# Kernel tuning notes

Hardware: AMD Instinct MI355X
Metric: run time of the kernel (lower is better)

Reference implementation:

```python
import jax, jax.numpy as jnp
import numpy as np

TOP_K = 2
UP = 4  # upfeat(disp_4, spg, 4, 4)


def reference(cost, spg):
    """cost: [b,1,D,h,w] raw cost volume; spg: [b,9,4h,4w] superpixel logits.
    Returns disp_1: [b,4h,4w] (eval-mode output of CoExDispProcessor regression)."""
    b, _, D, h, w = cost.shape
    # spx_pred = softmax over the 9 neighbor channels
    prob = jax.nn.softmax(spg, axis=1)  # [b,9,4h,4w]

    # --- topkpool (k=2): sort desc along disparity, take top-k values+indices ---
    c = jnp.moveaxis(cost, 2, -1)  # [b,1,h,w,D]
    vals, ind = jax.lax.top_k(c, TOP_K)  # [b,1,h,w,k], sorted descending
    corr = jax.nn.softmax(vals, axis=-1)
    disp4 = jnp.sum(corr * ind.astype(cost.dtype), axis=-1)  # [b,1,h,w]

    pad = jnp.pad(disp4, ((0, 0), (0, 0), (1, 1), (1, 1)))
    # F.unfold ordering: kernel row-major, channel index = ki*3 + kj
    patches = jnp.stack(
        [pad[:, 0, i:i + h, j:j + w] for i in range(3) for j in range(3)],
        axis=1)  # [b,9,h,w]
    up = jnp.repeat(jnp.repeat(patches, UP, axis=2), UP, axis=3)  # [b,9,4h,4w]
    disp1 = jnp.sum(up * prob, axis=1) * 4.0  # [b,4h,4w], scaled to full-res disparity
    return disp1


def setup_inputs() -> dict:
    key = jax.random.key(0)
    k1, k2 = jax.random.split(key)
    b, D, h, w = 8, 48, 128, 240
    cost = jax.random.normal(k1, (b, 1, D, h, w), dtype=jnp.float32)
    spg = jax.random.normal(k2, (b, 9, 4 * h, 4 * w), dtype=jnp.float32)
    return {"cost": cost, "spg": spg}
```

## Files before the change

### kernel.cpp

```cpp
#include <hip/hip_runtime.h>
#include <math.h>

#define BB 8
#define DD 48
#define HH 128
#define WW 240
#define HW (HH * WW)
#define FH (4 * HH)
#define FW (4 * WW)
#define FHW (FH * FW)

__global__ __launch_bounds__(256) void disp4_kernel(const float* __restrict__ cost,
                                                    float* __restrict__ disp4) {
    int t = blockIdx.x * blockDim.x + threadIdx.x;
    const int WQ = WW / 4;
    if (t >= BB * HH * WQ) return;
    int wq = t % WQ;
    int r  = t / WQ;
    int hy = r % HH;
    int b  = r / HH;

    const float* base = cost + (size_t)b * DD * HW + (size_t)hy * WW + wq * 4;

    float m1[4], m2[4], i1[4], i2[4];
#pragma unroll
    for (int k = 0; k < 4; ++k) { m1[k] = -INFINITY; m2[k] = -INFINITY; i1[k] = 0.f; i2[k] = 0.f; }

    for (int d = 0; d < DD; ++d) {
        float4 v4 = *reinterpret_cast<const float4*>(base + (size_t)d * HW);
        float v[4] = {v4.x, v4.y, v4.z, v4.w};
        float fd = (float)d;
#pragma unroll
        for (int k = 0; k < 4; ++k) {
            if (v[k] > m1[k]) {
                m2[k] = m1[k]; i2[k] = i1[k];
                m1[k] = v[k];  i1[k] = fd;
            } else if (v[k] > m2[k]) {
                m2[k] = v[k];  i2[k] = fd;
            }
        }
    }

    float4 o;
    float out[4];
#pragma unroll
    for (int k = 0; k < 4; ++k) {
        float e = __expf(m2[k] - m1[k]);
        float s = e / (1.f + e);
        out[k] = i1[k] + (i2[k] - i1[k]) * s;
    }
    o.x = out[0]; o.y = out[1]; o.z = out[2]; o.w = out[3];
    *reinterpret_cast<float4*>(disp4 + (size_t)b * HW + (size_t)hy * WW + wq * 4) = o;
}

__global__ __launch_bounds__(256) void upfeat_kernel(const float* __restrict__ spg,
                                                     const float* __restrict__ disp4,
                                                     float* __restrict__ out) {
    int t = blockIdx.x * blockDim.x + threadIdx.x;
    const int XQ = FW / 4;
    if (t >= BB * FH * XQ) return;
    int xq = t % XQ;
    int r  = t / XQ;
    int y  = r % FH;
    int b  = r / FH;
    int hy = y >> 2;

    float p[9];
#pragma unroll
    for (int i = 0; i < 3; ++i) {
#pragma unroll
        for (int j = 0; j < 3; ++j) {
            int cy = hy + i - 1;
            int cx = xq + j - 1;
            bool ok = (cy >= 0) & (cy < HH) & (cx >= 0) & (cx < WW);
            p[i * 3 + j] = ok ? disp4[(size_t)b * HW + (size_t)cy * WW + cx] : 0.f;
        }
    }

    const float* sp = spg + ((size_t)b * 9 * FH + (size_t)y) * FW + xq * 4;
    float s[9][4];
#pragma unroll
    for (int c = 0; c < 9; ++c) {
        float4 v = *reinterpret_cast<const float4*>(sp + (size_t)c * FHW);
        s[c][0] = v.x; s[c][1] = v.y; s[c][2] = v.z; s[c][3] = v.w;
    }

    float o[4];
#pragma unroll
    for (int k = 0; k < 4; ++k) {
        float m = s[0][k];
#pragma unroll
        for (int c = 1; c < 9; ++c) m = fmaxf(m, s[c][k]);
        float num = 0.f, den = 0.f;
#pragma unroll
        for (int c = 0; c < 9; ++c) {
            float e = __expf(s[c][k] - m);
            num = fmaf(e, p[c], num);
            den += e;
        }
        o[k] = 4.f * num / den;
    }

    float4 ov; ov.x = o[0]; ov.y = o[1]; ov.z = o[2]; ov.w = o[3];
    *reinterpret_cast<float4*>(out + ((size_t)b * FH + (size_t)y) * FW + xq * 4) = ov;
}

extern "C" void kernel_launch(void* const* d_in, const int* in_sizes, int n_in,
                              void* d_out, int out_size, void* d_ws, size_t ws_size,
                              hipStream_t stream) {
    const float* cost = (const float*)d_in[0];
    const float* spg  = (const float*)d_in[1];
    float* outp  = (float*)d_out;
    float* disp4 = (float*)d_ws;

    {
        int total = BB * HH * (WW / 4);
        int blocks = (total + 255) / 256;
        disp4_kernel<<<blocks, 256, 0, stream>>>(cost, disp4);
    }
    {
        int total = BB * FH * (FW / 4);
        int blocks = (total + 255) / 256;
        upfeat_kernel<<<blocks, 256, 0, stream>>>(spg, disp4, outp);
    }
}
```

Measured before the change: 258.8 us.

## Use nontemporal loads/stores, 2-wide topk threads with unrolled batched loads

The top-2 kernel now gives each thread two columns instead of four, doubling thread count, and unrolls the disparity loop in groups of eight, issuing all loads first and then doing branchless select updates. Both kernels switch to nontemporal loads, and the upsample kernel also uses a nontemporal store and a fast divide. The aim is more memory-level parallelism and less cache pollution on this bandwidth-bound streaming workload. Risks include narrower 8-byte loads and slightly less precise division.

```diff
diff --git a/kernel.cpp b/kernel.cpp
--- a/kernel.cpp
+++ b/kernel.cpp
@@ -10,47 +10,56 @@
 #define FW (4 * WW)
 #define FHW (FH * FW)
 
+typedef float vf2 __attribute__((ext_vector_type(2)));
+typedef float vf4 __attribute__((ext_vector_type(4)));
+
 __global__ __launch_bounds__(256) void disp4_kernel(const float* __restrict__ cost,
                                                     float* __restrict__ disp4) {
     int t = blockIdx.x * blockDim.x + threadIdx.x;
-    const int WQ = WW / 4;
+    const int WQ = WW / 2;
     if (t >= BB * HH * WQ) return;
     int wq = t % WQ;
     int r  = t / WQ;
     int hy = r % HH;
     int b  = r / HH;
 
-    const float* base = cost + (size_t)b * DD * HW + (size_t)hy * WW + wq * 4;
+    const float* base = cost + (size_t)b * DD * HW + (size_t)hy * WW + wq * 2;
 
-    float m1[4], m2[4], i1[4], i2[4];
+    float m1[2], m2[2], i1[2], i2[2];
 #pragma unroll
-    for (int k = 0; k < 4; ++k) { m1[k] = -INFINITY; m2[k] = -INFINITY; i1[k] = 0.f; i2[k] = 0.f; }
+    for (int k = 0; k < 2; ++k) { m1[k] = -INFINITY; m2[k] = -INFINITY; i1[k] = 0.f; i2[k] = 0.f; }
 
-    for (int d = 0; d < DD; ++d) {
-        float4 v4 = *reinterpret_cast<const float4*>(base + (size_t)d * HW);
-        float v[4] = {v4.x, v4.y, v4.z, v4.w};
-        float fd = (float)d;
 #pragma unroll
-        for (int k = 0; k < 4; ++k) {
-            if (v[k] > m1[k]) {
-                m2[k] = m1[k]; i2[k] = i1[k];
-                m1[k] = v[k];  i1[k] = fd;
-            } else if (v[k] > m2[k]) {
-                m2[k] = v[k];  i2[k] = fd;
+    for (int dd = 0; dd < DD; dd += 8) {
+        vf2 v[8];
+#pragma unroll
+        for (int u = 0; u < 8; ++u)
+            v[u] = __builtin_nontemporal_load(
+                reinterpret_cast<const vf2*>(base + (size_t)(dd + u) * HW));
+#pragma unroll
+        for (int u = 0; u < 8; ++u) {
+            float fd = (float)(dd + u);
+            float vv[2] = {v[u].x, v[u].y};
+#pragma unroll
+            for (int k = 0; k < 2; ++k) {
+                bool g1 = vv[k] > m1[k];
+                bool g2 = vv[k] > m2[k];
+                m2[k] = g1 ? m1[k] : (g2 ? vv[k] : m2[k]);
+                i2[k] = g1 ? i1[k] : (g2 ? fd    : i2[k]);
+                m1[k] = g1 ? vv[k] : m1[k];
+                i1[k] = g1 ? fd    : i1[k];
             }
         }
     }
 
-    float4 o;
-    float out[4];
+    vf2 o;
 #pragma unroll
-    for (int k = 0; k < 4; ++k) {
+    for (int k = 0; k < 2; ++k) {
         float e = __expf(m2[k] - m1[k]);
         float s = e / (1.f + e);
-        out[k] = i1[k] + (i2[k] - i1[k]) * s;
+        o[k] = i1[k] + (i2[k] - i1[k]) * s;
     }
-    o.x = out[0]; o.y = out[1]; o.z = out[2]; o.w = out[3];
-    *reinterpret_cast<float4*>(disp4 + (size_t)b * HW + (size_t)hy * WW + wq * 4) = o;
+    *reinterpret_cast<vf2*>(disp4 + (size_t)b * HW + (size_t)hy * WW + wq * 2) = o;
 }
 
 __global__ __launch_bounds__(256) void upfeat_kernel(const float* __restrict__ spg,
@@ -81,11 +90,12 @@
     float s[9][4];
 #pragma unroll
     for (int c = 0; c < 9; ++c) {
-        float4 v = *reinterpret_cast<const float4*>(sp + (size_t)c * FHW);
+        vf4 v = __builtin_nontemporal_load(
+            reinterpret_cast<const vf4*>(sp + (size_t)c * FHW));
         s[c][0] = v.x; s[c][1] = v.y; s[c][2] = v.z; s[c][3] = v.w;
     }
 
-    float o[4];
+    vf4 ov;
 #pragma unroll
     for (int k = 0; k < 4; ++k) {
         float m = s[0][k];
@@ -98,11 +108,11 @@
             num = fmaf(e, p[c], num);
             den += e;
         }
-        o[k] = 4.f * num / den;
+        ov[k] = 4.f * __fdividef(num, den);
     }
 
-    float4 ov; ov.x = o[0]; ov.y = o[1]; ov.z = o[2]; ov.w = o[3];
-    *reinterpret_cast<float4*>(out + ((size_t)b * FH + (size_t)y) * FW + xq * 4) = ov;
+    __builtin_nontemporal_store(ov, reinterpret_cast<vf4*>(
+        out + ((size_t)b * FH + (size_t)y) * FW + xq * 4));
 }
 
 extern "C" void kernel_launch(void* const* d_in, const int* in_sizes, int n_in,
@@ -114,7 +124,7 @@
     float* disp4 = (float*)d_ws;
 
     {
-        int total = BB * HH * (WW / 4);
+        int total = BB * HH * (WW / 2);
         int blocks = (total + 255) / 256;
         disp4_kernel<<<blocks, 256, 0, stream>>>(cost, disp4);
     }
```

After: 218.4 us. 1.18x faster.
